# Kernel tuning notes

Measured on AMD Instinct MI355X. Metric: run time of the kernel, lower is better.

The kernel has to match this reference:

```python
import math
import jax, jax.numpy as jnp
import numpy as np

ALPHA, BETA, GAMMA = 1.9, 3.8, 15.2
HEIGHT, WIDTH, SKIP = 32, 32, 1
NUM_HEADS, DIM = 12, 768
HEAD_DIM = DIM // NUM_HEADS


def _piecewise_index_np(rp, alpha, beta, gamma):
    # Eq. (18): identity inside |rp|<=alpha, logarithmic bucketing outside, clipped at beta.
    rp = rp.astype(np.float64)
    rp_abs = np.abs(rp)
    inside = np.round(rp)
    log_part = alpha + np.log(np.maximum(rp_abs, 1e-9) / alpha) / math.log(gamma / alpha) * (beta - alpha)
    outside = np.sign(rp) * np.minimum(np.round(log_part), beta)
    return np.where(rp_abs <= alpha, inside, outside).astype(np.int64)


def _bucket_ids_cross(height, width, skip, alpha, beta, gamma, axis):
    # axis=0 -> CROSS_ROWS, axis=1 -> CROSS_COLS
    rows = np.arange(height)[:, None].repeat(width, 1)
    cols = np.arange(width)[None, :].repeat(height, 0)
    pos = np.stack([rows, cols], 2).reshape(-1, 2)  # [L, 2]
    diff = pos[:, None, axis] - pos[None, :, axis]  # [L, L]
    beta_int = int(beta)
    ids = _piecewise_index_np(diff, alpha, beta, gamma) + beta_int  # in [0, 2*beta_int]
    num_buckets = 2 * beta_int + 1
    L = height * width
    if skip > 0:
        extra = num_buckets
        new_ids = np.full((skip + L, skip + L), extra, dtype=np.int64)
        new_ids[skip:, skip:] = ids
        ids = new_ids
        num_buckets += 1
    return ids.astype(np.int32), num_buckets


def setup_inputs() -> dict:
    key = jax.random.key(0)
    ks = jax.random.split(key, 8)
    N = SKIP + HEIGHT * WIDTH  # 1025
    B = 8
    br, nb = _bucket_ids_cross(HEIGHT, WIDTH, SKIP, ALPHA, BETA, GAMMA, axis=0)
    bc, _ = _bucket_ids_cross(HEIGHT, WIDTH, SKIP, ALPHA, BETA, GAMMA, axis=1)
    w = 0.02
    return {
        "x": jax.random.normal(ks[0], (B, N, DIM), jnp.float32),
        "qkv_w": jax.random.normal(ks[1], (3 * DIM, DIM), jnp.float32) * w,
        "qkv_b": jnp.zeros((3 * DIM,), jnp.float32),
        "proj_w": jax.random.normal(ks[2], (DIM, DIM), jnp.float32) * w,
        "proj_b": jnp.zeros((DIM,), jnp.float32),
        "rpe_rows": jax.random.normal(ks[3], (NUM_HEADS, nb, HEAD_DIM), jnp.float32) * w,
        "rpe_cols": jax.random.normal(ks[4], (NUM_HEADS, nb, HEAD_DIM), jnp.float32) * w,
        "bucket_rows": jnp.asarray(br),
        "bucket_cols": jnp.asarray(bc),
    }


def reference(x, qkv_w, qkv_b, proj_w, proj_b, rpe_rows, rpe_cols, bucket_rows, bucket_cols):
    B, N, C = x.shape
    h = rpe_rows.shape[0]
    d = C // h
    scale = d ** -0.5
    qkv = (x @ qkv_w.T + qkv_b).reshape(B, N, 3, h, d).transpose(2, 0, 3, 1, 4)  # [3,B,h,N,d]
    q, k, v = qkv[0] * scale, qkv[1], qkv[2]
    attn = jnp.einsum('bhid,bhjd->bhij', q, k)  # [B,h,N,N]
    # contextual RPE on keys: project q onto per-head bucket tables, gather per (i,j)
    qt_r = jnp.einsum('bhid,hud->bhiu', q, rpe_rows)  # [B,h,N,nb]
    qt_c = jnp.einsum('bhid,hud->bhiu', q, rpe_cols)
    bias = (jnp.take_along_axis(qt_r, bucket_rows[None, None].astype(jnp.int32), axis=3)
            + jnp.take_along_axis(qt_c, bucket_cols[None, None].astype(jnp.int32), axis=3))
    attn = jax.nn.softmax(attn + bias, axis=-1)
    out = jnp.einsum('bhij,bhjd->bhid', attn, v)
    out = out.transpose(0, 2, 1, 3).reshape(B, N, C)
    return out @ proj_w.T + proj_b
```

## Files before the change

### kernel.cpp

```cpp
#include <hip/hip_runtime.h>
#include <hip/hip_bf16.h>

typedef unsigned short u16;
typedef unsigned int   u32;
typedef short  s16x8 __attribute__((ext_vector_type(8)));
typedef float  f32x4 __attribute__((ext_vector_type(4)));

#define B_   8
#define N_   1025
#define H_   12
#define D_   64
#define C_   768
#define NB_  8
#define M_   (B_*N_)
#define QKV_ (3*C_)
#define NEGI -30000.0f
#define LOG2E 1.44269504089f
#define SHIFT2 11.5415603271f
#define CS_  1088

__device__ __forceinline__ float bf2f(u16 u) {
    unsigned int i = ((unsigned int)u) << 16;
    float f; __builtin_memcpy(&f, &i, 4); return f;
}
__device__ __forceinline__ u16 f2bf(float f) {
    __hip_bfloat16 h = __float2bfloat16(f);
    u16 u; __builtin_memcpy(&u, &h, 2); return u;
}
__device__ __forceinline__ float exp2fast(float x) {
#if __has_builtin(__builtin_amdgcn_exp2f)
    return __builtin_amdgcn_exp2f(x);
#else
    float r; asm("v_exp_f32 %0, %1" : "=v"(r) : "v"(x)); return r;
#endif
}

__device__ __forceinline__ void gload_lds16(const u16* gptr, u16* lptr) {
    __builtin_amdgcn_global_load_lds(
        (const __attribute__((address_space(1))) void*)gptr,
        (__attribute__((address_space(3))) void*)lptr, 16, 0, 0);
}

__global__ __launch_bounds__(256)
void cvt_f32_bf16(const float* __restrict__ a, u16* __restrict__ oa, long na,
                  const float* __restrict__ b, u16* __restrict__ ob, long nb,
                  const float* __restrict__ c, u16* __restrict__ oc, long nc)
{
    long t = ((long)blockIdx.x * 256 + threadIdx.x) * 8;
    const float* s; u16* d; long off;
    if (t < na)                 { s = a; d = oa; off = t; }
    else if (t < na + nb)       { s = b; d = ob; off = t - na; }
    else if (t < na + nb + nc)  { s = c; d = oc; off = t - na - nb; }
    else return;
    float4 f0 = *reinterpret_cast<const float4*>(s + off);
    float4 f1 = *reinterpret_cast<const float4*>(s + off + 4);
    u16 tmp[8] = { f2bf(f0.x), f2bf(f0.y), f2bf(f0.z), f2bf(f0.w),
                   f2bf(f1.x), f2bf(f1.y), f2bf(f1.z), f2bf(f1.w) };
    *reinterpret_cast<uint4*>(d + off) = *reinterpret_cast<uint4*>(tmp);
}

__global__ void build_cidx(const int* __restrict__ brow, const int* __restrict__ bcol,
                           unsigned char* __restrict__ cidx) {
    long t = (long)blockIdx.x * 256 + threadIdx.x;
    const long total = (long)CS_ * (CS_ / 4);
    if (t >= total) return;
    int i = (int)(t / (CS_ / 4));
    int k = (int)(t % (CS_ / 4));
    u32 w = 0;
    int p0 = k * 4;
    #pragma unroll
    for (int bnb = 0; bnb < 4; ++bnb) {
        int p = p0 + bnb;
        int jt = p >> 6, rem = p & 63;
        int l = rem >> 2, bn = rem & 3;
        int j = jt * 64 + bn * 16 + l;
        u32 c = 63u;
        if (i < N_ && j < N_) {
            u32 br = (u32)(brow[(size_t)i * N_ + j] & 7);
            u32 bc = (u32)(bcol[(size_t)i * N_ + j] & 7);
            c = (br << 3) | bc;
        }
        w |= c << (8 * bnb);
    }
    ((u32*)cidx)[t] = w;
}

template<int OF32>
__global__ __launch_bounds__(256)
void gemm_bt(const u16* __restrict__ Ap, int lda,
             const u16* __restrict__ Btp,
             const float* __restrict__ bias,
             void* __restrict__ Cout, int ldc,
             int M, int Nn, int K, int scale_cols, float scale_val)
{
    __shared__ u16 As[128][64];
    __shared__ u16 Bs[128][64];
    const int tid  = threadIdx.x;
    const int lane = tid & 63;
    const int wave = tid >> 6;
    const int wm = (wave >> 1) * 64;
    const int wn = (wave & 1) * 64;
    const int m0 = blockIdx.y * 128;
    const int n0 = blockIdx.x * 128;

    const int srow = wave * 32 + (lane >> 3);
    const int gcol = (((lane & 7) ^ ((lane >> 3) & 7))) * 8;

    f32x4 acc[4][4] = {};

    for (int k0 = 0; k0 < K; k0 += 64) {
        __syncthreads();
        #pragma unroll
        for (int i = 0; i < 4; ++i) {
            int ar = m0 + srow + i * 8;
            if (ar > M - 1) ar = M - 1;
            gload_lds16(Ap + (size_t)ar * lda + k0 + gcol, &As[wave * 32 + i * 8][0]);
            int br = n0 + srow + i * 8;
            gload_lds16(Btp + (size_t)br * K + k0 + gcol,  &Bs[wave * 32 + i * 8][0]);
        }
        __syncthreads();

        #pragma unroll
        for (int kk = 0; kk < 2; ++kk) {
            const int kc = ((kk * 4 + (lane >> 4)) ^ (lane & 7)) << 3;
            s16x8 af[4], bfv[4];
            #pragma unroll
            for (int qq = 0; qq < 4; ++qq) {
                af[qq]  = *reinterpret_cast<const s16x8*>(&As[wm + qq*16 + (lane & 15)][kc]);
                bfv[qq] = *reinterpret_cast<const s16x8*>(&Bs[wn + qq*16 + (lane & 15)][kc]);
            }
            #pragma unroll
            for (int bm = 0; bm < 4; ++bm)
                #pragma unroll
                for (int bn = 0; bn < 4; ++bn)
                    acc[bm][bn] = __builtin_amdgcn_mfma_f32_16x16x32_bf16(af[bm], bfv[bn], acc[bm][bn], 0, 0, 0);
        }
    }

    #pragma unroll
    for (int bm = 0; bm < 4; ++bm) {
        #pragma unroll
        for (int bn = 0; bn < 4; ++bn) {
            int col = n0 + wn + bn*16 + (lane & 15);
            float bv = bias[col];
            float sc = (col < scale_cols) ? scale_val : 1.0f;
            #pragma unroll
            for (int r = 0; r < 4; ++r) {
                int row = m0 + wm + bm*16 + (lane >> 4)*4 + r;
                if (row < M) {
                    float v = (acc[bm][bn][r] + bv) * sc;
                    size_t idx = (size_t)row * ldc + col;
                    if (OF32) ((float*)Cout)[idx] = v;
                    else      ((u16*)Cout)[idx]   = f2bf(v);
                }
            }
        }
    }
}

__global__ __launch_bounds__(512, 4)
void flash_kernel(const u16* __restrict__ qkv,
                  const float* __restrict__ rpe_r, const float* __restrict__ rpe_c,
                  const unsigned char* __restrict__ cidx,
                  u16* __restrict__ aout)
{
    __shared__ u16 Ks[64][64];
    __shared__ u16 Vt[64][72];
    __shared__ u16 Ps[8][16][72];
    __shared__ float qtCombF[128][68];

    const int tid  = threadIdx.x;
    const int lane = tid & 63;
    const int wave = tid >> 6;
    const int q    = lane >> 4;
    const int l    = lane & 15;

    const int L   = blockIdx.x;
    const int xcd = L & 7;
    const int s_  = L >> 3;
    const int bh  = xcd + 8 * (s_ / 9);
    const int bx  = s_ % 9;
    const int b = bh / H_;
    const int h = bh % H_;
    const int i0 = bx * 128;
    const bool wactive = (i0 + wave * 16) < N_;

    float* qtrA = (float*)&Ps[0][0][0];
    float* qtcA = qtrA + 128 * 8;

    {
        int row = tid >> 2;
        int u0  = (tid & 3) * 2;
        int ig = i0 + row;
        bool valid = ig < N_;
        const u16* qrow = &qkv[(size_t)(b * N_ + (valid ? ig : 0)) * QKV_ + h * D_];
        #pragma unroll
        for (int uu = 0; uu < 2; ++uu) {
            int u = u0 + uu;
            const float4* rr4 = (const float4*)&rpe_r[(size_t)(h * NB_ + u) * D_];
            const float4* rc4 = (const float4*)&rpe_c[(size_t)(h * NB_ + u) * D_];
            float sr = 0.f, sc = 0.f;
            #pragma unroll
            for (int e2 = 0; e2 < 8; ++e2) {
                uint4 t = *reinterpret_cast<const uint4*>(&qrow[e2 * 8]);
                s16x8 q8 = *reinterpret_cast<s16x8*>(&t);
                float4 a0 = rr4[2*e2], a1 = rr4[2*e2+1];
                float4 c0 = rc4[2*e2], c1 = rc4[2*e2+1];
                float f0 = bf2f((u16)q8[0]), f1 = bf2f((u16)q8[1]);
                float f2 = bf2f((u16)q8[2]), f3 = bf2f((u16)q8[3]);
                float f4 = bf2f((u16)q8[4]), f5 = bf2f((u16)q8[5]);
                float f6 = bf2f((u16)q8[6]), f7 = bf2f((u16)q8[7]);
                sr += f0*a0.x + f1*a0.y + f2*a0.z + f3*a0.w
                    + f4*a1.x + f5*a1.y + f6*a1.z + f7*a1.w;
                sc += f0*c0.x + f1*c0.y + f2*c0.z + f3*c0.w
                    + f4*c1.x + f5*c1.y + f6*c1.z + f7*c1.w;
            }
            qtrA[row*8 + u] = valid ? sr : 0.f;
            qtcA[row*8 + u] = valid ? sc : 0.f;
        }
    }
    __syncthreads();
    {
        int row = tid >> 2;
        int c0  = (tid & 3) * 16;
        float tmp[16];
        #pragma unroll
        for (int cc = 0; cc < 16; ++cc) {
            int c = c0 + cc;
            tmp[cc] = qtrA[row*8 + (c >> 3)] + qtcA[row*8 + (c & 7)];
        }
        #pragma unroll
        for (int v4 = 0; v4 < 4; ++v4)
            *reinterpret_cast<float4*>(&qtCombF[row][c0 + v4 * 4]) =
                *reinterpret_cast<float4*>(&tmp[v4 * 4]);
    }

    s16x8 qf[2];
    {
        int iq = i0 + wave * 16 + l;
        #pragma unroll
        for (int ks = 0; ks < 2; ++ks) {
            uint4 v = make_uint4(0u, 0u, 0u, 0u);
            if (iq < N_)
                v = *reinterpret_cast<const uint4*>(
                    &qkv[(size_t)(b * N_ + iq) * QKV_ + h * D_ + ks * 32 + q * 8]);
            qf[ks] = *reinterpret_cast<s16x8*>(&v);
        }
    }

    float l_part[4] = {0.f, 0.f, 0.f, 0.f};
    f32x4 o_acc[4] = {};

    const int srow = tid >> 3;
    const int g8   = tid & 7;
    const int scol = g8 * 8;
    const int sgc  = ((tid & 7) ^ ((tid >> 3) & 7)) * 8;
    const int rowq  = wave * 16 + q * 4;
    const int rowq4 = q * 4;

    uint4 vpre;
    {
        gload_lds16(qkv + (size_t)(b * N_ + srow) * QKV_ + C_ + h * D_ + sgc,
                    &Ks[wave * 8][0]);
        size_t base = (size_t)(b * N_ + srow) * QKV_ + h * D_ + scol;
        vpre = *reinterpret_cast<const uint4*>(&qkv[base + 2 * C_]);
    }

#define SMAX_BN(bn, MASKED_)                                                  \
    {                                                                         \
        const int jbw = (((bn) << 1) | (l >> 3)) ^ q;                         \
        const int sw = (jbw << 3) | (l & 7);                                  \
        _Pragma("unroll")                                                     \
        for (int r = 0; r < 4; ++r) {                                         \
            int c = (cpk[r] >> ((bn) * 8)) & 63;                              \
            float biasv = qtCombF[rowq + r][c];                               \
            float lg = s[bn][r] + biasv;                                      \
            if (MASKED_) { if ((j0 + (bn) * 16 + l) >= N_) lg = NEGI; }       \
            float p = exp2fast(lg);                                           \
            l_part[r] += p;                                                   \
            Ps[wave][rowq4 + r][sw] = f2bf(p);                                \
        }                                                                     \
    }

#define PVHALF(ks)                                                            \
    {                                                                         \
        const int qi = (l >> 2) & 3;                                          \
        s16x8 pf = *reinterpret_cast<const s16x8*>(                           \
            &Ps[wave][l][((((ks) << 2) | q) ^ qi) << 3]);                     \
        __builtin_amdgcn_s_setprio(1);                                        \
        _Pragma("unroll")                                                     \
        for (int bn = 0; bn < 4; ++bn) {                                      \
            int gd = ((bn << 1) | (l >> 3)) & 7;                              \
            int jb = (((ks) << 2) | q) ^ gd;                                  \
            s16x8 vf = *reinterpret_cast<const s16x8*>(&Vt[bn * 16 + l][jb << 3]); \
            o_acc[bn] = __builtin_amdgcn_mfma_f32_16x16x32_bf16(pf, vf, o_acc[bn], 0, 0, 0); \
        }                                                                     \
        __builtin_amdgcn_s_setprio(0);                                        \
    }

    const int nJT = (N_ + 63) / 64;
    for (int jt = 0; jt < nJT; ++jt) {
        const int j0 = jt * 64;

        __syncthreads();

        u32 cpk[4];
        if (wactive) {
            #pragma unroll
            for (int r = 0; r < 4; ++r) {
                int ig = i0 + wave * 16 + q * 4 + r;
                if (ig > CS_ - 1) ig = CS_ - 1;
                cpk[r] = *reinterpret_cast<const u32*>(&cidx[(size_t)ig * CS_ + j0 + 4 * l]);
            }
        }

        {
            s16x8 v8 = *reinterpret_cast<s16x8*>(&vpre);
            int base = (((srow >> 3) ^ g8) << 3) | (srow & 7);
            #pragma unroll
            for (int e = 0; e < 8; ++e) Vt[scol + e][base] = (u16)v8[e];
        }

        f32x4 s[4];
        if (wactive) {
            #pragma unroll
            for (int bn = 0; bn < 4; ++bn)
                s[bn] = (f32x4){-SHIFT2, -SHIFT2, -SHIFT2, -SHIFT2};
            __builtin_amdgcn_s_setprio(1);
            #pragma unroll
            for (int bn = 0; bn < 4; ++bn) {
                #pragma unroll
                for (int ks = 0; ks < 2; ++ks) {
                    s16x8 kf = *reinterpret_cast<const s16x8*>(
                        &Ks[bn * 16 + l][(((ks * 4 + q) ^ (l & 7)) << 3)]);
                    s[bn] = __builtin_amdgcn_mfma_f32_16x16x32_bf16(qf[ks], kf, s[bn], 0, 0, 0);
                }
            }
            __builtin_amdgcn_s_setprio(0);
        }

        __syncthreads();

        if (jt + 1 < nJT) {
            int jg = j0 + 64 + srow;
            int jk = (jg > N_ - 1) ? (N_ - 1) : jg;
            gload_lds16(qkv + (size_t)(b * N_ + jk) * QKV_ + C_ + h * D_ + sgc,
                        &Ks[wave * 8][0]);
            vpre = make_uint4(0u, 0u, 0u, 0u);
            if (jg < N_) {
                size_t base = (size_t)(b * N_ + jg) * QKV_ + h * D_ + scol;
                vpre = *reinterpret_cast<const uint4*>(&qkv[base + 2 * C_]);
            }
        }

        if (wactive) {
            if (jt < nJT - 1) {
                SMAX_BN(0, 0) SMAX_BN(1, 0)
                PVHALF(0)
                SMAX_BN(2, 0) SMAX_BN(3, 0)
                PVHALF(1)
            } else {
                SMAX_BN(0, 1) SMAX_BN(1, 1)
                PVHALF(0)
                SMAX_BN(2, 1) SMAX_BN(3, 1)
                PVHALF(1)
            }
        }
    }

    #pragma unroll
    for (int r = 0; r < 4; ++r) {
        #pragma unroll
        for (int s2 = 1; s2 < 16; s2 <<= 1)
            l_part[r] += __shfl_xor(l_part[r], s2, 64);
    }
    #pragma unroll
    for (int bn = 0; bn < 4; ++bn) {
        #pragma unroll
        for (int r = 0; r < 4; ++r) {
            int ig = i0 + wave * 16 + q * 4 + r;
            if (ig < N_) {
                float lsum = l_part[r];
                float invl = (lsum > 0.f) ? (1.0f / lsum) : 0.f;
                aout[(size_t)(b * N_ + ig) * C_ + h * D_ + bn * 16 + l] = f2bf(o_acc[bn][r] * invl);
            }
        }
    }
#undef SMAX_BN
#undef PVHALF
}

extern "C" void kernel_launch(void* const* d_in, const int* in_sizes, int n_in,
                              void* d_out, int out_size, void* d_ws, size_t ws_size,
                              hipStream_t stream)
{
    const float* x      = (const float*)d_in[0];
    const float* qkv_w  = (const float*)d_in[1];
    const float* qkv_b  = (const float*)d_in[2];
    const float* proj_w = (const float*)d_in[3];
    const float* proj_b = (const float*)d_in[4];
    const float* rpe_r  = (const float*)d_in[5];
    const float* rpe_c  = (const float*)d_in[6];
    const int*   brow   = (const int*)d_in[7];
    const int*   bcol   = (const int*)d_in[8];

    char* p = (char*)d_ws;
    u16* qkv  = (u16*)p; p += (size_t)M_ * QKV_ * 2;
    u16* xaout = (u16*)p; p += (size_t)M_ * C_ * 2;
    unsigned char* cidx = (unsigned char*)p; p += (size_t)CS_ * CS_;
    u16* w1bf = (u16*)p; p += (size_t)QKV_ * C_ * 2;
    u16* w2bf = (u16*)p;

    const long nx = (long)M_ * C_;
    const long n1 = (long)QKV_ * C_;
    const long n2 = (long)C_ * C_;

    cvt_f32_bf16<<<(int)((nx + n1 + n2) / 8 / 256), 256, 0, stream>>>(
        x, xaout, nx, qkv_w, w1bf, n1, proj_w, w2bf, n2);

    build_cidx<<<((CS_ * (CS_ / 4)) + 255) / 256, 256, 0, stream>>>(brow, bcol, cidx);

    gemm_bt<0><<<dim3(QKV_ / 128, (M_ + 127) / 128), 256, 0, stream>>>(
        xaout, C_, w1bf, qkv_b, qkv, QKV_, M_, QKV_, C_, C_, 0.125f * LOG2E);

    flash_kernel<<<dim3(8 * 12 * 9), 512, 0, stream>>>(
        qkv, rpe_r, rpe_c, cidx, xaout);

    gemm_bt<1><<<dim3(C_ / 128, (M_ + 127) / 128), 256, 0, stream>>>(
        xaout, C_, w2bf, proj_b, d_out, C_, M_, C_, C_, 0, 1.0f);
}
```

Baseline: 299.3 us.

## Double-buffer K/V tiles in LDS and store bias table as bf16

K and V tiles now alternate between two LDS buffers, so the next tile is stored and prefetched before the current QK^T runs. This drops the mid-iteration __syncthreads that used to separate compute from the next load, and the V global prefetch now runs two tiles ahead. To pay for the extra LDS, the combined RPE bias table is kept as bf16 instead of fp32, which adds rounding error to the logits.

New measurement: 305.1 us. Within noise of the previous version (+1.9%).

```diff
diff --git a/kernel.cpp b/kernel.cpp
--- a/kernel.cpp
+++ b/kernel.cpp
@@ -164,10 +164,10 @@
                   const unsigned char* __restrict__ cidx,
                   u16* __restrict__ aout)
 {
-    __shared__ u16 Ks[64][64];
-    __shared__ u16 Vt[64][72];
+    __shared__ u16 Ks[2][64][64];
+    __shared__ u16 Vt[2][64][72];
     __shared__ u16 Ps[8][16][72];
-    __shared__ float qtCombF[128][68];
+    __shared__ u16 qtComb[128][68];
 
     const int tid  = threadIdx.x;
     const int lane = tid & 63;
@@ -223,16 +223,14 @@
     {
         int row = tid >> 2;
         int c0  = (tid & 3) * 16;
-        float tmp[16];
+        u16 tmp[16];
         #pragma unroll
         for (int cc = 0; cc < 16; ++cc) {
             int c = c0 + cc;
-            tmp[cc] = qtrA[row*8 + (c >> 3)] + qtcA[row*8 + (c & 7)];
-        }
-        #pragma unroll
-        for (int v4 = 0; v4 < 4; ++v4)
-            *reinterpret_cast<float4*>(&qtCombF[row][c0 + v4 * 4]) =
-                *reinterpret_cast<float4*>(&tmp[v4 * 4]);
+            tmp[cc] = f2bf(qtrA[row*8 + (c >> 3)] + qtcA[row*8 + (c & 7)]);
+        }
+        *reinterpret_cast<uint4*>(&qtComb[row][c0])     = *reinterpret_cast<uint4*>(&tmp[0]);
+        *reinterpret_cast<uint4*>(&qtComb[row][c0 + 8]) = *reinterpret_cast<uint4*>(&tmp[8]);
     }
 
     s16x8 qf[2];
@@ -255,15 +253,21 @@
     const int g8   = tid & 7;
     const int scol = g8 * 8;
     const int sgc  = ((tid & 7) ^ ((tid >> 3) & 7)) * 8;
+    const int vbase = (((srow >> 3) ^ g8) << 3) | (srow & 7);
     const int rowq  = wave * 16 + q * 4;
     const int rowq4 = q * 4;
 
     uint4 vpre;
     {
+        size_t base0 = (size_t)(b * N_ + srow) * QKV_ + h * D_ + scol;
+        uint4 v0 = *reinterpret_cast<const uint4*>(&qkv[base0 + 2 * C_]);
+        s16x8 v8 = *reinterpret_cast<s16x8*>(&v0);
+        #pragma unroll
+        for (int e = 0; e < 8; ++e) Vt[0][scol + e][vbase] = (u16)v8[e];
         gload_lds16(qkv + (size_t)(b * N_ + srow) * QKV_ + C_ + h * D_ + sgc,
-                    &Ks[wave * 8][0]);
-        size_t base = (size_t)(b * N_ + srow) * QKV_ + h * D_ + scol;
-        vpre = *reinterpret_cast<const uint4*>(&qkv[base + 2 * C_]);
+                    &Ks[0][wave * 8][0]);
+        size_t base1 = (size_t)(b * N_ + 64 + srow) * QKV_ + h * D_ + scol;
+        vpre = *reinterpret_cast<const uint4*>(&qkv[base1 + 2 * C_]);
     }
 
 #define SMAX_BN(bn, MASKED_)                                                  \
@@ -273,7 +277,7 @@
         _Pragma("unroll")                                                     \
         for (int r = 0; r < 4; ++r) {                                         \
             int c = (cpk[r] >> ((bn) * 8)) & 63;                              \
-            float biasv = qtCombF[rowq + r][c];                               \
+            float biasv = bf2f(qtComb[rowq + r][c]);                          \
             float lg = s[bn][r] + biasv;                                      \
             if (MASKED_) { if ((j0 + (bn) * 16 + l) >= N_) lg = NEGI; }       \
             float p = exp2fast(lg);                                           \
@@ -292,15 +296,17 @@
         for (int bn = 0; bn < 4; ++bn) {                                      \
             int gd = ((bn << 1) | (l >> 3)) & 7;                              \
             int jb = (((ks) << 2) | q) ^ gd;                                  \
-            s16x8 vf = *reinterpret_cast<const s16x8*>(&Vt[bn * 16 + l][jb << 3]); \
+            s16x8 vf = *reinterpret_cast<const s16x8*>(&VtC[bn * 16 + l][jb << 3]); \
             o_acc[bn] = __builtin_amdgcn_mfma_f32_16x16x32_bf16(pf, vf, o_acc[bn], 0, 0, 0); \
         }                                                                     \
         __builtin_amdgcn_s_setprio(0);                                        \
     }
 
     const int nJT = (N_ + 63) / 64;
+    int cur = 0;
     for (int jt = 0; jt < nJT; ++jt) {
         const int j0 = jt * 64;
+        const int nxt = cur ^ 1;
 
         __syncthreads();
 
@@ -314,11 +320,14 @@
             }
         }
 
-        {
+        if (jt + 1 < nJT) {
             s16x8 v8 = *reinterpret_cast<s16x8*>(&vpre);
-            int base = (((srow >> 3) ^ g8) << 3) | (srow & 7);
-            #pragma unroll
-            for (int e = 0; e < 8; ++e) Vt[scol + e][base] = (u16)v8[e];
+            #pragma unroll
+            for (int e = 0; e < 8; ++e) Vt[nxt][scol + e][vbase] = (u16)v8[e];
+            int jg = j0 + 64 + srow;
+            int jk = (jg > N_ - 1) ? (N_ - 1) : jg;
+            gload_lds16(qkv + (size_t)(b * N_ + jk) * QKV_ + C_ + h * D_ + sgc,
+                        &Ks[nxt][wave * 8][0]);
         }
 
         f32x4 s[4];
@@ -332,20 +341,15 @@
                 #pragma unroll
                 for (int ks = 0; ks < 2; ++ks) {
                     s16x8 kf = *reinterpret_cast<const s16x8*>(
-                        &Ks[bn * 16 + l][(((ks * 4 + q) ^ (l & 7)) << 3)]);
+                        &Ks[cur][bn * 16 + l][(((ks * 4 + q) ^ (l & 7)) << 3)]);
                     s[bn] = __builtin_amdgcn_mfma_f32_16x16x32_bf16(qf[ks], kf, s[bn], 0, 0, 0);
                 }
             }
             __builtin_amdgcn_s_setprio(0);
         }
 
-        __syncthreads();
-
-        if (jt + 1 < nJT) {
-            int jg = j0 + 64 + srow;
-            int jk = (jg > N_ - 1) ? (N_ - 1) : jg;
-            gload_lds16(qkv + (size_t)(b * N_ + jk) * QKV_ + C_ + h * D_ + sgc,
-                        &Ks[wave * 8][0]);
+        if (jt + 2 < nJT) {
+            int jg = j0 + 128 + srow;
             vpre = make_uint4(0u, 0u, 0u, 0u);
             if (jg < N_) {
                 size_t base = (size_t)(b * N_ + jg) * QKV_ + h * D_ + scol;
@@ -354,6 +358,7 @@
         }
 
         if (wactive) {
+            u16 (*VtC)[72] = Vt[cur];
             if (jt < nJT - 1) {
                 SMAX_BN(0, 0) SMAX_BN(1, 0)
                 PVHALF(0)
@@ -366,6 +371,7 @@
                 PVHALF(1)
             }
         }
+        cur = nxt;
     }
 
     #pragma unroll
```

## Write V transposed from QKV GEMM epilogue and double-buffer V tiles via direct LDS loads

Applied to the files above, without the earlier changes.

The QKV GEMM epilogue now writes V into a separate pre-transposed [B,H,D,N] buffer padded to 1088 columns, while Q and K stay in a narrower row-major buffer. The flash kernel then loads V tiles straight into a double-buffered LDS array with async global-to-LDS loads, replacing the register prefetch and per-element scatter transpose into LDS. The aim is to remove LDS transpose work and bank conflicts from the attention inner loop and to overlap V loads with compute. In exchange, the GEMM epilogue's V stores become strided and uncoalesced, an extra kernel zeroes the padding, and LDS use grows.

After: 317.2 us. 6.0% more time.

```diff
diff --git a/kernel.cpp b/kernel.cpp
--- a/kernel.cpp
+++ b/kernel.cpp
@@ -14,6 +14,8 @@
 #define NB_  8
 #define M_   (B_*N_)
 #define QKV_ (3*C_)
+#define QK2_ 1536
+#define VS2_ 1088
 #define NEGI -30000.0f
 #define LOG2E 1.44269504089f
 #define SHIFT2 11.5415603271f
@@ -57,6 +59,16 @@
     u16 tmp[8] = { f2bf(f0.x), f2bf(f0.y), f2bf(f0.z), f2bf(f0.w),
                    f2bf(f1.x), f2bf(f1.y), f2bf(f1.z), f2bf(f1.w) };
     *reinterpret_cast<uint4*>(d + off) = *reinterpret_cast<uint4*>(tmp);
+}
+
+__global__ __launch_bounds__(256)
+void zero_vpad(u16* __restrict__ vT) {
+    const int pad = VS2_ - N_;
+    int t = blockIdx.x * 256 + threadIdx.x;
+    const int total = B_ * H_ * D_ * pad;
+    if (t >= total) return;
+    int rr = t / pad, pp = t % pad;
+    vT[(size_t)rr * VS2_ + N_ + pp] = 0;
 }
 
 __global__ void build_cidx(const int* __restrict__ brow, const int* __restrict__ bcol,
@@ -85,13 +97,14 @@
     ((u32*)cidx)[t] = w;
 }
 
-template<int OF32>
+template<int OF32, int VT>
 __global__ __launch_bounds__(256)
 void gemm_bt(const u16* __restrict__ Ap, int lda,
              const u16* __restrict__ Btp,
              const float* __restrict__ bias,
              void* __restrict__ Cout, int ldc,
-             int M, int Nn, int K, int scale_cols, float scale_val)
+             int M, int Nn, int K, int scale_cols, float scale_val,
+             u16* __restrict__ vt)
 {
     __shared__ u16 As[128][64];
     __shared__ u16 Bs[128][64];
@@ -149,9 +162,16 @@
                 int row = m0 + wm + bm*16 + (lane >> 4)*4 + r;
                 if (row < M) {
                     float v = (acc[bm][bn][r] + bv) * sc;
-                    size_t idx = (size_t)row * ldc + col;
-                    if (OF32) ((float*)Cout)[idx] = v;
-                    else      ((u16*)Cout)[idx]   = f2bf(v);
+                    if (VT && col >= 2 * C_) {
+                        int b2 = row / N_;
+                        int j2 = row - b2 * N_;
+                        int hd = col - 2 * C_;
+                        vt[((size_t)(b2 * (H_ * D_) + hd)) * VS2_ + j2] = f2bf(v);
+                    } else {
+                        size_t idx = (size_t)row * ldc + col;
+                        if (OF32) ((float*)Cout)[idx] = v;
+                        else      ((u16*)Cout)[idx]   = f2bf(v);
+                    }
                 }
             }
         }
@@ -160,12 +180,13 @@
 
 __global__ __launch_bounds__(512, 4)
 void flash_kernel(const u16* __restrict__ qkv,
+                  const u16* __restrict__ vT,
                   const float* __restrict__ rpe_r, const float* __restrict__ rpe_c,
                   const unsigned char* __restrict__ cidx,
                   u16* __restrict__ aout)
 {
     __shared__ u16 Ks[64][64];
-    __shared__ u16 Vt[64][72];
+    __shared__ u16 Vt[2][64][64];
     __shared__ u16 Ps[8][16][72];
     __shared__ float qtCombF[128][68];
 
@@ -185,6 +206,15 @@
     const int i0 = bx * 128;
     const bool wactive = (i0 + wave * 16) < N_;
 
+    const int srow = tid >> 3;
+    const int sgc  = ((tid & 7) ^ ((tid >> 3) & 7)) * 8;
+
+    const u16* kbase = qkv + (size_t)b * N_ * QK2_ + C_ + h * D_;
+    const u16* vbase = vT + ((size_t)(b * H_ + h) * D_ + srow) * VS2_;
+
+    gload_lds16(kbase + (size_t)srow * QK2_ + sgc, &Ks[wave * 8][0]);
+    gload_lds16(vbase + 0 + sgc,                   &Vt[0][wave * 8][0]);
+
     float* qtrA = (float*)&Ps[0][0][0];
     float* qtcA = qtrA + 128 * 8;
 
@@ -193,7 +223,7 @@
         int u0  = (tid & 3) * 2;
         int ig = i0 + row;
         bool valid = ig < N_;
-        const u16* qrow = &qkv[(size_t)(b * N_ + (valid ? ig : 0)) * QKV_ + h * D_];
+        const u16* qrow = &qkv[(size_t)(b * N_ + (valid ? ig : 0)) * QK2_ + h * D_];
         #pragma unroll
         for (int uu = 0; uu < 2; ++uu) {
             int u = u0 + uu;
@@ -243,7 +273,7 @@
             uint4 v = make_uint4(0u, 0u, 0u, 0u);
             if (iq < N_)
                 v = *reinterpret_cast<const uint4*>(
-                    &qkv[(size_t)(b * N_ + iq) * QKV_ + h * D_ + ks * 32 + q * 8]);
+                    &qkv[(size_t)(b * N_ + iq) * QK2_ + h * D_ + ks * 32 + q * 8]);
             qf[ks] = *reinterpret_cast<s16x8*>(&v);
         }
     }
@@ -251,20 +281,8 @@
     float l_part[4] = {0.f, 0.f, 0.f, 0.f};
     f32x4 o_acc[4] = {};
 
-    const int srow = tid >> 3;
-    const int g8   = tid & 7;
-    const int scol = g8 * 8;
-    const int sgc  = ((tid & 7) ^ ((tid >> 3) & 7)) * 8;
     const int rowq  = wave * 16 + q * 4;
     const int rowq4 = q * 4;
-
-    uint4 vpre;
-    {
-        gload_lds16(qkv + (size_t)(b * N_ + srow) * QKV_ + C_ + h * D_ + sgc,
-                    &Ks[wave * 8][0]);
-        size_t base = (size_t)(b * N_ + srow) * QKV_ + h * D_ + scol;
-        vpre = *reinterpret_cast<const uint4*>(&qkv[base + 2 * C_]);
-    }
 
 #define SMAX_BN(bn, MASKED_)                                                  \
     {                                                                         \
@@ -290,17 +308,18 @@
         __builtin_amdgcn_s_setprio(1);                                        \
         _Pragma("unroll")                                                     \
         for (int bn = 0; bn < 4; ++bn) {                                      \
-            int gd = ((bn << 1) | (l >> 3)) & 7;                              \
-            int jb = (((ks) << 2) | q) ^ gd;                                  \
-            s16x8 vf = *reinterpret_cast<const s16x8*>(&Vt[bn * 16 + l][jb << 3]); \
+            s16x8 vf = *reinterpret_cast<const s16x8*>(                       \
+                &VtC[bn * 16 + l][((((ks) * 4 + q) ^ (l & 7)) << 3)]);        \
             o_acc[bn] = __builtin_amdgcn_mfma_f32_16x16x32_bf16(pf, vf, o_acc[bn], 0, 0, 0); \
         }                                                                     \
         __builtin_amdgcn_s_setprio(0);                                        \
     }
 
     const int nJT = (N_ + 63) / 64;
+    int cur = 0;
     for (int jt = 0; jt < nJT; ++jt) {
         const int j0 = jt * 64;
+        const int nxt = cur ^ 1;
 
         __syncthreads();
 
@@ -312,13 +331,6 @@
                 if (ig > CS_ - 1) ig = CS_ - 1;
                 cpk[r] = *reinterpret_cast<const u32*>(&cidx[(size_t)ig * CS_ + j0 + 4 * l]);
             }
-        }
-
-        {
-            s16x8 v8 = *reinterpret_cast<s16x8*>(&vpre);
-            int base = (((srow >> 3) ^ g8) << 3) | (srow & 7);
-            #pragma unroll
-            for (int e = 0; e < 8; ++e) Vt[scol + e][base] = (u16)v8[e];
         }
 
         f32x4 s[4];
@@ -344,16 +356,12 @@
         if (jt + 1 < nJT) {
             int jg = j0 + 64 + srow;
             int jk = (jg > N_ - 1) ? (N_ - 1) : jg;
-            gload_lds16(qkv + (size_t)(b * N_ + jk) * QKV_ + C_ + h * D_ + sgc,
-                        &Ks[wave * 8][0]);
-            vpre = make_uint4(0u, 0u, 0u, 0u);
-            if (jg < N_) {
-                size_t base = (size_t)(b * N_ + jg) * QKV_ + h * D_ + scol;
-                vpre = *reinterpret_cast<const uint4*>(&qkv[base + 2 * C_]);
-            }
+            gload_lds16(kbase + (size_t)jk * QK2_ + sgc, &Ks[wave * 8][0]);
+            gload_lds16(vbase + j0 + 64 + sgc,           &Vt[nxt][wave * 8][0]);
         }
 
         if (wactive) {
+            u16 (*VtC)[64] = Vt[cur];
             if (jt < nJT - 1) {
                 SMAX_BN(0, 0) SMAX_BN(1, 0)
                 PVHALF(0)
@@ -366,6 +374,7 @@
                 PVHALF(1)
             }
         }
+        cur = nxt;
     }
 
     #pragma unroll
@@ -405,8 +414,9 @@
     const int*   bcol   = (const int*)d_in[8];
 
     char* p = (char*)d_ws;
-    u16* qkv  = (u16*)p; p += (size_t)M_ * QKV_ * 2;
+    u16* qkv2  = (u16*)p; p += (size_t)M_ * QK2_ * 2;
     u16* xaout = (u16*)p; p += (size_t)M_ * C_ * 2;
+    u16* vT    = (u16*)p; p += (size_t)B_ * H_ * D_ * VS2_ * 2;
     unsigned char* cidx = (unsigned char*)p; p += (size_t)CS_ * CS_;
     u16* w1bf = (u16*)p; p += (size_t)QKV_ * C_ * 2;
     u16* w2bf = (u16*)p;
@@ -418,14 +428,15 @@
     cvt_f32_bf16<<<(int)((nx + n1 + n2) / 8 / 256), 256, 0, stream>>>(
         x, xaout, nx, qkv_w, w1bf, n1, proj_w, w2bf, n2);
 
+    zero_vpad<<<(B_ * H_ * D_ * (VS2_ - N_) + 255) / 256, 256, 0, stream>>>(vT);
     build_cidx<<<((CS_ * (CS_ / 4)) + 255) / 256, 256, 0, stream>>>(brow, bcol, cidx);
 
-    gemm_bt<0><<<dim3(QKV_ / 128, (M_ + 127) / 128), 256, 0, stream>>>(
-        xaout, C_, w1bf, qkv_b, qkv, QKV_, M_, QKV_, C_, C_, 0.125f * LOG2E);
+    gemm_bt<0,1><<<dim3(QKV_ / 128, (M_ + 127) / 128), 256, 0, stream>>>(
+        xaout, C_, w1bf, qkv_b, qkv2, QK2_, M_, QKV_, C_, C_, 0.125f * LOG2E, vT);
 
     flash_kernel<<<dim3(8 * 12 * 9), 512, 0, stream>>>(
-        qkv, rpe_r, rpe_c, cidx, xaout);
-
-    gemm_bt<1><<<dim3(C_ / 128, (M_ + 127) / 128), 256, 0, stream>>>(
-        xaout, C_, w2bf, proj_b, d_out, C_, M_, C_, C_, 0, 1.0f);
-}
+        qkv2, vT, rpe_r, rpe_c, cidx, xaout);
+
+    gemm_bt<1,0><<<dim3(C_ / 128, (M_ + 127) / 128), 256, 0, stream>>>(
+        xaout, C_, w2bf, proj_b, d_out, C_, M_, C_, C_, 0, 1.0f, nullptr);
+}
```
